# Performance work log

Measured on AMD Instinct MI355X. Metric: run time of the kernel, lower is better.

The kernel has to match this reference:

```python
import jax, jax.numpy as jnp
import numpy as np

RATIO = 10.0
MAXPOOL_K = 101   # local-max window (samples)
MED_K = 6000      # MAD window (samples)
MED_STRIDE = MED_K // 2
TOP_K = 100


def setup_inputs() -> dict:
    key = jax.random.key(0)
    xcorr = jax.random.normal(key, (2, 3, 16, 360000), dtype=jnp.float32)
    return {"xcorr": xcorr}


def _detect(xcorr):
    nb, nc, nx, nt = xcorr.shape
    neg = jnp.finfo(xcorr.dtype).min
    # max_pool2d kernel (1, 101), stride 1, pad (0, 50) -> local sliding max over time
    smax = jax.lax.reduce_window(
        xcorr, neg, jax.lax.max,
        (1, 1, 1, MAXPOOL_K), (1, 1, 1, 1),
        [(0, 0), (0, 0), (0, 0), (MAXPOOL_K // 2, MAXPOOL_K // 2)])
    # reflect-pad right by MED_K then unfold(size=MED_K, stride=MED_STRIDE)
    padded = jnp.pad(xcorr, ((0, 0), (0, 0), (0, 0), (0, MED_K)), mode='reflect')
    nblocks = (nt + MED_K) // MED_STRIDE  # exact by construction
    blocks = padded.reshape(nb, nc, nx, nblocks, MED_STRIDE)
    # each window = two consecutive half-overlapping blocks -> [nb,nc,nx,nw,MED_K]
    windows = jnp.concatenate([blocks[..., :-1, :], blocks[..., 1:, :]], axis=-1)
    mid = (MED_K - 1) // 2  # torch.median returns lower median for even n
    med = jnp.sort(windows, axis=-1)[..., mid]
    mad = jnp.sort(jnp.abs(windows - med[..., None]), axis=-1)[..., mid]  # [nb,nc,nx,nw]
    # bilinear interpolate along time by scale MED_STRIDE (align_corners=False), crop to nt
    in_w = mad.shape[-1]
    pos = (jnp.arange(nt, dtype=jnp.float32) + 0.5) / MED_STRIDE - 0.5
    pos = jnp.maximum(pos, 0.0)
    x0 = jnp.minimum(jnp.floor(pos).astype(jnp.int32), in_w - 1)
    x1 = jnp.minimum(x0 + 1, in_w - 1)
    w = pos - x0.astype(jnp.float32)
    mad_t = mad[..., x0] * (1.0 - w) + mad[..., x1] * w  # [nb,nc,nx,nt]
    # keep local maxima exceeding ratio * MAD, zero the rest, then top-k per trace
    keep = (smax == xcorr) & (xcorr > RATIO * mad_t)
    masked = xcorr * keep.astype(xcorr.dtype)
    topk_scores, topk_inds = jax.lax.top_k(masked, TOP_K)
    return topk_scores, topk_inds


def reference(xcorr):
    return _detect(xcorr)
```

## Files before the change

### kernel.cpp

```cpp
#include <hip/hip_runtime.h>
#include <stdint.h>

#define NT      360000
#define NTRACE  96
#define MEDK    6000
#define MSTRIDE 3000
#define NW      121
#define HALFW   50
#define TOPK    100
#define DETCAP  128
#define RATIO_F 10.0f
#define DCHUNKS 12
#define CAP     2304

__device__ __forceinline__ uint32_t f2key(float f) {
    uint32_t u = __float_as_uint(f);
    return u ^ (uint32_t)(((int32_t)u >> 31) | 0x80000000);
}
__device__ __forceinline__ float key2f(uint32_t k) {
    uint32_t u = (k & 0x80000000u) ? (k & 0x7fffffffu) : ~k;
    return __uint_as_float(u);
}

struct SelShared {
    uint32_t hist[1024];
    uint32_t cmp[CAP];
    uint32_t segtot[4];
    uint32_t s_bin, s_rank, s_cnt, ccount;
};

__device__ void bin_select(SelShared* sh, uint32_t rank)
{
    const int tid  = threadIdx.x;
    const int lane = tid & 63;
    const int wv   = tid >> 6;
    uint32_t c = sh->hist[tid] + sh->hist[256 + tid] +
                 sh->hist[512 + tid] + sh->hist[768 + tid];
    uint32_t incl = c;
    #pragma unroll
    for (int off = 1; off < 64; off <<= 1) {
        uint32_t v = __shfl_up(incl, off);
        if (lane >= off) incl += v;
    }
    if (lane == 63) sh->segtot[wv] = incl;
    __syncthreads();
    uint32_t segoff = 0;
    for (int j = 0; j < wv; ++j) segoff += sh->segtot[j];
    incl += segoff;
    uint32_t excl = incl - c;
    if (rank > excl && rank <= incl) {
        sh->s_bin = (uint32_t)tid; sh->s_rank = rank - excl; sh->s_cnt = c;
    }
    __syncthreads();
}

__device__ float select_rank3000(const float* ls, float sub, bool useabs,
                                 SelShared* sh)
{
    const int tid = threadIdx.x;
    const int wv  = tid >> 6;
    uint32_t* myhist = &sh->hist[wv * 256];

    for (int i = tid; i < 1024; i += 256) sh->hist[i] = 0;
    if (tid == 0) sh->ccount = 0;
    __syncthreads();
    for (int i = tid; i < MEDK / 4; i += 256) {
        float4 v4 = ((const float4*)ls)[i];
        float vv[4] = {v4.x, v4.y, v4.z, v4.w};
        #pragma unroll
        for (int e = 0; e < 4; ++e) {
            float v = vv[e];
            if (useabs) v = fabsf(v - sub);
            atomicAdd(&myhist[f2key(v) >> 24], 1u);
        }
    }
    __syncthreads();
    bin_select(sh, 3000u);
    const uint32_t b0 = sh->s_bin, cnt = sh->s_cnt;
    uint32_t rank   = sh->s_rank;
    uint32_t prefix = b0 << 24;
    uint32_t pmask  = 0xFF000000u;
    const bool usec = (cnt <= CAP);

    if (usec) {
        for (int i = tid; i < MEDK / 4; i += 256) {
            float4 v4 = ((const float4*)ls)[i];
            float vv[4] = {v4.x, v4.y, v4.z, v4.w};
            #pragma unroll
            for (int e = 0; e < 4; ++e) {
                float v = vv[e];
                if (useabs) v = fabsf(v - sub);
                uint32_t k = f2key(v);
                if ((k >> 24) == b0) {
                    uint32_t p = atomicAdd(&sh->ccount, 1u);
                    sh->cmp[p] = k;
                }
            }
        }
        __syncthreads();
    }

    for (int pass = 1; pass < 4; ++pass) {
        const int shift = 24 - 8 * pass;
        for (int i = tid; i < 1024; i += 256) sh->hist[i] = 0;
        __syncthreads();
        if (usec) {
            for (int i = tid; i < (int)cnt; i += 256) {
                uint32_t k = sh->cmp[i];
                if ((k & pmask) == prefix)
                    atomicAdd(&myhist[(k >> shift) & 0xFFu], 1u);
            }
        } else {
            for (int i = tid; i < MEDK / 4; i += 256) {
                float4 v4 = ((const float4*)ls)[i];
                float vv[4] = {v4.x, v4.y, v4.z, v4.w};
                #pragma unroll
                for (int e = 0; e < 4; ++e) {
                    float v = vv[e];
                    if (useabs) v = fabsf(v - sub);
                    uint32_t k = f2key(v);
                    if ((k & pmask) == prefix)
                        atomicAdd(&myhist[(k >> shift) & 0xFFu], 1u);
                }
            }
        }
        __syncthreads();
        bin_select(sh, rank);
        prefix |= sh->s_bin << shift;
        pmask  |= 0xFFu << shift;
        rank    = sh->s_rank;
        __syncthreads();
    }
    return key2f(prefix);
}

__global__ __launch_bounds__(256) void mad_kernel(const float* __restrict__ x,
                                                  float* __restrict__ mad)
{
    __shared__ float     ls[MEDK];
    __shared__ SelShared sh;
    const int tr = blockIdx.x / NW;
    const int w  = blockIdx.x % NW;
    const float* xt = x + (size_t)tr * NT;
    const int t0 = w * MSTRIDE;
    if (t0 + MEDK <= NT) {
        const float4* src4 = (const float4*)(xt + t0);
        float4* dst4 = (float4*)ls;
        for (int i = threadIdx.x; i < MEDK / 4; i += 256) dst4[i] = src4[i];
    } else {
        for (int i = threadIdx.x; i < MEDK; i += 256) {
            int g = t0 + i;
            int src = (g < NT) ? g : (2 * NT - 2 - g);
            ls[i] = xt[src];
        }
    }
    __syncthreads();
    float med  = select_rank3000(ls, 0.0f, false, &sh);
    __syncthreads();
    float madv = select_rank3000(ls, med,  true,  &sh);
    if (threadIdx.x == 0) mad[tr * NW + w] = madv;
}

__global__ __launch_bounds__(256) void detect_kernel(const float* __restrict__ x,
                                                     const float* __restrict__ mad,
                                                     uint32_t* __restrict__ counters,
                                                     uint64_t* __restrict__ det)
{
    __shared__ float smad[NW];
    const int tr = blockIdx.x / DCHUNKS;
    const int ch = blockIdx.x % DCHUNKS;
    const float* xt = x + (size_t)tr * NT;
    for (int i = threadIdx.x; i < NW; i += 256) smad[i] = mad[tr * NW + i];
    __syncthreads();
    const int tbeg = ch * (NT / DCHUNKS);
    const int tend = tbeg + (NT / DCHUNKS);
    for (int t = tbeg + threadIdx.x * 4; t < tend; t += 256 * 4) {
        float4 v4 = *(const float4*)(xt + t);
        float vv[4] = {v4.x, v4.y, v4.z, v4.w};
        #pragma unroll
        for (int k = 0; k < 4; ++k) {
            int   tt = t + k;
            float v  = vv[k];
            float pos = ((float)tt + 0.5f) / (float)MSTRIDE - 0.5f;
            pos = fmaxf(pos, 0.0f);
            int   x0 = min((int)floorf(pos), NW - 1);
            int   x1 = min(x0 + 1, NW - 1);
            float wg = pos - (float)x0;
            float m  = smad[x0] * (1.0f - wg) + smad[x1] * wg;
            if (v > RATIO_F * m) {
                bool ismax = true;
                int lo = max(tt - HALFW, 0), hi = min(tt + HALFW, NT - 1);
                for (int j = lo; j <= hi && ismax; ++j) ismax = (xt[j] <= v);
                if (ismax) {
                    uint32_t slot = atomicAdd(&counters[tr], 1u);
                    if (slot < DETCAP)
                        det[(size_t)tr * DETCAP + slot] =
                            ((uint64_t)f2key(v) << 32) | (uint32_t)(~(uint32_t)tt);
                }
            }
        }
    }
}

__global__ __launch_bounds__(64) void finalize_kernel(const float* __restrict__ x,
                                                      const uint32_t* __restrict__ counters,
                                                      const uint64_t* __restrict__ det,
                                                      float* __restrict__ out)
{
    __shared__ uint64_t sdet[DETCAP];
    __shared__ int sposs[TOPK];
    __shared__ int snegs[TOPK];
    __shared__ int s_np, s_nn;
    const int tr   = blockIdx.x;
    const int lane = threadIdx.x;
    const int D = (int)min(counters[tr], (uint32_t)DETCAP);
    for (int i = lane; i < D; i += 64) sdet[i] = det[(size_t)tr * DETCAP + i];
    if (lane == 0) { s_np = 0; s_nn = 0; }
    __syncthreads();

    const float* xt = x + (size_t)tr * NT;
    for (int base = 0; base < NT; base += 64) {
        int np0 = s_np, nn0 = s_nn;
        if (np0 >= TOPK && nn0 >= TOPK) break;
        int  t     = base + lane;
        bool valid = (t < NT);
        uint32_t bits = valid ? __float_as_uint(xt[t]) : 0u;
        bool nonneg = valid && !(bits >> 31);
        bool neg    = valid &&  (bits >> 31);
        if (nonneg && D > 0) {
            for (int i = 0; i < D; ++i) {
                int dt = (int)(~(uint32_t)(sdet[i] & 0xFFFFFFFFull));
                if (dt == t) { nonneg = false; break; }
            }
        }
        unsigned long long bp = __ballot(nonneg);
        unsigned long long bn = __ballot(neg);
        unsigned long long below = (1ull << lane) - 1ull;
        int pidx = np0 + __popcll(bp & below);
        int nidx = nn0 + __popcll(bn & below);
        if (nonneg && pidx < TOPK) sposs[pidx] = t;
        if (neg    && nidx < TOPK) snegs[nidx] = t;
        __syncthreads();
        if (lane == 0) { s_np = np0 + __popcll(bp); s_nn = nn0 + __popcll(bn); }
        __syncthreads();
    }
    __syncthreads();

    if (lane == 0) {
        for (int i = 1; i < D; ++i) {
            uint64_t k = sdet[i]; int j = i - 1;
            while (j >= 0 && sdet[j] < k) { sdet[j + 1] = sdet[j]; --j; }
            sdet[j + 1] = k;
        }
    }
    __syncthreads();

    const int nd   = min(D, TOPK);
    const int npos = min(s_np, TOPK);
    float* oscore = out + (size_t)tr * TOPK;
    float* oidx   = out + (size_t)NTRACE * TOPK + (size_t)tr * TOPK;
    for (int j = lane; j < TOPK; j += 64) {
        float sc; int idx;
        if (j < nd) {
            uint64_t k = sdet[j];
            sc  = key2f((uint32_t)(k >> 32));
            idx = (int)(~(uint32_t)(k & 0xFFFFFFFFull));
        } else if (j - nd < npos) {
            sc = 0.0f;  idx = sposs[j - nd];
        } else {
            int jj = j - nd - npos;
            sc = -0.0f; idx = (jj < TOPK) ? snegs[jj] : 0;
        }
        oscore[j] = sc;
        oidx[j]   = (float)idx;
    }
}

extern "C" void kernel_launch(void* const* d_in, const int* in_sizes, int n_in,
                              void* d_out, int out_size, void* d_ws, size_t ws_size,
                              hipStream_t stream)
{
    const float* x = (const float*)d_in[0];
    float* out = (float*)d_out;
    char* ws = (char*)d_ws;
    float*    mad      = (float*)ws;
    uint32_t* counters = (uint32_t*)(ws + 46464);
    uint64_t* det      = (uint64_t*)(ws + 46464 + 384);

    hipMemsetAsync(counters, 0, NTRACE * sizeof(uint32_t), stream);
    hipLaunchKernelGGL(mad_kernel,    dim3(NTRACE * NW),      dim3(256), 0, stream, x, mad);
    hipLaunchKernelGGL(detect_kernel, dim3(NTRACE * DCHUNKS), dim3(256), 0, stream, x, mad, counters, det);
    hipLaunchKernelGGL(finalize_kernel, dim3(NTRACE),         dim3(64),  0, stream, x, counters, det, out);
}
```

Baseline: 550.4 us.

## Keep MAD windows in registers, widen histogram copies, aggregate compaction atomics

The MAD kernel now holds each 6000-sample window in per-thread float4 registers instead of a shared-memory buffer. This frees LDS for higher occupancy (launch bounds 5) and removes shared-memory reads on every histogram pass. Histograms use 8 padded copies (one per half-wave) to cut atomic contention and bank conflicts. Candidate compaction uses wave-level ballot aggregation instead of one atomic per element. The detect kernel doubles its chunk count and prefetches the next float4, trading more register pressure for parallelism and latency hiding.

```diff
diff --git a/kernel.cpp b/kernel.cpp
--- a/kernel.cpp
+++ b/kernel.cpp
@@ -10,8 +10,11 @@
 #define TOPK    100
 #define DETCAP  128
 #define RATIO_F 10.0f
-#define DCHUNKS 12
+#define DCHUNKS 24
 #define CAP     2304
+#define NCOPY   8
+#define HSTRIDE 257
+#define NSLOT   6
 
 __device__ __forceinline__ uint32_t f2key(float f) {
     uint32_t u = __float_as_uint(f);
@@ -23,7 +26,7 @@
 }
 
 struct SelShared {
-    uint32_t hist[1024];
+    uint32_t hist[NCOPY * HSTRIDE];
     uint32_t cmp[CAP];
     uint32_t segtot[4];
     uint32_t s_bin, s_rank, s_cnt, ccount;
@@ -34,8 +37,9 @@
     const int tid  = threadIdx.x;
     const int lane = tid & 63;
     const int wv   = tid >> 6;
-    uint32_t c = sh->hist[tid] + sh->hist[256 + tid] +
-                 sh->hist[512 + tid] + sh->hist[768 + tid];
+    uint32_t c = 0;
+    #pragma unroll
+    for (int j = 0; j < NCOPY; ++j) c += sh->hist[j * HSTRIDE + tid];
     uint32_t incl = c;
     #pragma unroll
     for (int off = 1; off < 64; off <<= 1) {
@@ -54,24 +58,32 @@
     __syncthreads();
 }
 
-__device__ float select_rank3000(const float* ls, float sub, bool useabs,
-                                 SelShared* sh)
-{
-    const int tid = threadIdx.x;
-    const int wv  = tid >> 6;
-    uint32_t* myhist = &sh->hist[wv * 256];
-
-    for (int i = tid; i < 1024; i += 256) sh->hist[i] = 0;
+__device__ __forceinline__ void zero_hist(SelShared* sh)
+{
+    uint4* h4 = (uint4*)sh->hist;
+    for (int i = threadIdx.x; i < 514; i += 256) h4[i] = make_uint4(0, 0, 0, 0);
+}
+
+__device__ float select_from_regs(const float4 (&r)[NSLOT], float sub, bool useabs,
+                                  SelShared* sh)
+{
+    const int tid  = threadIdx.x;
+    const int lane = tid & 63;
+    uint32_t* myhist = &sh->hist[(tid >> 5) * HSTRIDE];
+
+    zero_hist(sh);
     if (tid == 0) sh->ccount = 0;
     __syncthreads();
-    for (int i = tid; i < MEDK / 4; i += 256) {
-        float4 v4 = ((const float4*)ls)[i];
-        float vv[4] = {v4.x, v4.y, v4.z, v4.w};
-        #pragma unroll
-        for (int e = 0; e < 4; ++e) {
-            float v = vv[e];
-            if (useabs) v = fabsf(v - sub);
-            atomicAdd(&myhist[f2key(v) >> 24], 1u);
+    #pragma unroll
+    for (int k = 0; k < NSLOT; ++k) {
+        if (k * 256 + tid < MEDK / 4) {
+            float vv[4] = {r[k].x, r[k].y, r[k].z, r[k].w};
+            #pragma unroll
+            for (int e = 0; e < 4; ++e) {
+                float v = vv[e];
+                if (useabs) v = fabsf(v - sub);
+                atomicAdd(&myhist[f2key(v) >> 24], 1u);
+            }
         }
     }
     __syncthreads();
@@ -83,17 +95,27 @@
     const bool usec = (cnt <= CAP);
 
     if (usec) {
-        for (int i = tid; i < MEDK / 4; i += 256) {
-            float4 v4 = ((const float4*)ls)[i];
-            float vv[4] = {v4.x, v4.y, v4.z, v4.w};
+        #pragma unroll
+        for (int k = 0; k < NSLOT; ++k) {
+            bool valid = (k * 256 + tid < MEDK / 4);
+            float vv[4] = {r[k].x, r[k].y, r[k].z, r[k].w};
             #pragma unroll
             for (int e = 0; e < 4; ++e) {
-                float v = vv[e];
-                if (useabs) v = fabsf(v - sub);
-                uint32_t k = f2key(v);
-                if ((k >> 24) == b0) {
-                    uint32_t p = atomicAdd(&sh->ccount, 1u);
-                    sh->cmp[p] = k;
+                uint32_t key = 0; bool m = false;
+                if (valid) {
+                    float v = vv[e];
+                    if (useabs) v = fabsf(v - sub);
+                    key = f2key(v);
+                    m = ((key >> 24) == b0);
+                }
+                unsigned long long b = __ballot(m);
+                if (b) {
+                    int leader = __ffsll((unsigned long long)b) - 1;
+                    uint32_t pcnt = (uint32_t)__popcll(b & ((1ull << lane) - 1ull));
+                    uint32_t wbase = 0;
+                    if (lane == leader) wbase = atomicAdd(&sh->ccount, (uint32_t)__popcll(b));
+                    wbase = __shfl(wbase, leader);
+                    if (m) sh->cmp[wbase + pcnt] = key;
                 }
             }
         }
@@ -102,7 +124,7 @@
 
     for (int pass = 1; pass < 4; ++pass) {
         const int shift = 24 - 8 * pass;
-        for (int i = tid; i < 1024; i += 256) sh->hist[i] = 0;
+        zero_hist(sh);
         __syncthreads();
         if (usec) {
             for (int i = tid; i < (int)cnt; i += 256) {
@@ -111,16 +133,18 @@
                     atomicAdd(&myhist[(k >> shift) & 0xFFu], 1u);
             }
         } else {
-            for (int i = tid; i < MEDK / 4; i += 256) {
-                float4 v4 = ((const float4*)ls)[i];
-                float vv[4] = {v4.x, v4.y, v4.z, v4.w};
-                #pragma unroll
-                for (int e = 0; e < 4; ++e) {
-                    float v = vv[e];
-                    if (useabs) v = fabsf(v - sub);
-                    uint32_t k = f2key(v);
-                    if ((k & pmask) == prefix)
-                        atomicAdd(&myhist[(k >> shift) & 0xFFu], 1u);
+            #pragma unroll
+            for (int k = 0; k < NSLOT; ++k) {
+                if (k * 256 + tid < MEDK / 4) {
+                    float vv[4] = {r[k].x, r[k].y, r[k].z, r[k].w};
+                    #pragma unroll
+                    for (int e = 0; e < 4; ++e) {
+                        float v = vv[e];
+                        if (useabs) v = fabsf(v - sub);
+                        uint32_t kk = f2key(v);
+                        if ((kk & pmask) == prefix)
+                            atomicAdd(&myhist[(kk >> shift) & 0xFFu], 1u);
+                    }
                 }
             }
         }
@@ -134,30 +158,43 @@
     return key2f(prefix);
 }
 
-__global__ __launch_bounds__(256) void mad_kernel(const float* __restrict__ x,
-                                                  float* __restrict__ mad)
-{
-    __shared__ float     ls[MEDK];
+__global__ __launch_bounds__(256, 5) void mad_kernel(const float* __restrict__ x,
+                                                     float* __restrict__ mad)
+{
     __shared__ SelShared sh;
     const int tr = blockIdx.x / NW;
     const int w  = blockIdx.x % NW;
     const float* xt = x + (size_t)tr * NT;
     const int t0 = w * MSTRIDE;
+
+    float4 r[NSLOT];
     if (t0 + MEDK <= NT) {
         const float4* src4 = (const float4*)(xt + t0);
-        float4* dst4 = (float4*)ls;
-        for (int i = threadIdx.x; i < MEDK / 4; i += 256) dst4[i] = src4[i];
+        #pragma unroll
+        for (int k = 0; k < NSLOT; ++k) {
+            int i4 = k * 256 + threadIdx.x;
+            r[k] = (i4 < MEDK / 4) ? src4[i4] : make_float4(0.f, 0.f, 0.f, 0.f);
+        }
     } else {
-        for (int i = threadIdx.x; i < MEDK; i += 256) {
-            int g = t0 + i;
-            int src = (g < NT) ? g : (2 * NT - 2 - g);
-            ls[i] = xt[src];
-        }
-    }
-    __syncthreads();
-    float med  = select_rank3000(ls, 0.0f, false, &sh);
-    __syncthreads();
-    float madv = select_rank3000(ls, med,  true,  &sh);
+        #pragma unroll
+        for (int k = 0; k < NSLOT; ++k) {
+            int i4 = k * 256 + threadIdx.x;
+            float tmp[4] = {0.f, 0.f, 0.f, 0.f};
+            if (i4 < MEDK / 4) {
+                #pragma unroll
+                for (int e = 0; e < 4; ++e) {
+                    int g = t0 + i4 * 4 + e;
+                    int src = (g < NT) ? g : (2 * NT - 2 - g);
+                    tmp[e] = xt[src];
+                }
+            }
+            r[k] = make_float4(tmp[0], tmp[1], tmp[2], tmp[3]);
+        }
+    }
+    __syncthreads();
+    float med  = select_from_regs(r, 0.0f, false, &sh);
+    __syncthreads();
+    float madv = select_from_regs(r, med,  true,  &sh);
     if (threadIdx.x == 0) mad[tr * NW + w] = madv;
 }
 
@@ -174,8 +211,14 @@
     __syncthreads();
     const int tbeg = ch * (NT / DCHUNKS);
     const int tend = tbeg + (NT / DCHUNKS);
-    for (int t = tbeg + threadIdx.x * 4; t < tend; t += 256 * 4) {
-        float4 v4 = *(const float4*)(xt + t);
+    const int stride = 256 * 4;
+    int t0 = tbeg + threadIdx.x * 4;
+    float4 nxt = (t0 < tend) ? *(const float4*)(xt + t0)
+                             : make_float4(0.f, 0.f, 0.f, 0.f);
+    for (int t = t0; t < tend; t += stride) {
+        float4 v4 = nxt;
+        int tn = t + stride;
+        if (tn < tend) nxt = *(const float4*)(xt + tn);
         float vv[4] = {v4.x, v4.y, v4.z, v4.w};
         #pragma unroll
         for (int k = 0; k < 4; ++k) {
```

Result: faster. 493.2 us (-10.4%).
